# Kernel tuning notes

Hardware: AMD Instinct MI355X
Metric: run time of the kernel (lower is better)

The kernel has to match this reference:

```python
import jax, jax.numpy as jnp
import numpy as np

FISTA_ITER = 50
LAMBDA = 0.1
POWER_ITER = 100


def power_method(W):
    # Estimates c = largest eigenvalue of W^T W (squared spectral norm).
    # Torch code uses a random init vector; we use a fixed key for determinism.
    X0 = jax.random.normal(jax.random.key(1), (1, W.shape[1]), dtype=W.dtype)

    def body(i, carry):
        X, _ = carry
        X = (X @ W.T) @ W            # [1, m]
        nm = jnp.linalg.norm(X)
        return (X / nm, nm)

    _, nm = jax.lax.fori_loop(0, POWER_ITER, body, (X0, jnp.asarray(1.0, W.dtype)))
    return nm


def soft_threshold(X, lam):
    return jnp.sign(X) * jax.nn.relu(jnp.abs(X) - lam)


def fista(Y, W, lam, iters):
    c = power_method(W)
    eta = 1.0 / c
    Gamma0 = soft_threshold(Y @ (eta * W), lam)   # [B, m]
    Y_norm = jnp.linalg.norm(Y)
    t0 = jnp.asarray(1.0, Y.dtype)

    def step(carry, _):
        Gamma, Z, t = carry
        residual = Z @ W.T - Y                                   # [B, n]
        Gamma_new = soft_threshold(Z - eta * (residual @ W), lam / c)
        t_new = (1.0 + jnp.sqrt(1.0 + 4.0 * t ** 2)) / 2.0
        Z_new = Gamma_new + (t - 1.0) / t_new * (Gamma_new - Gamma)
        nrm = jnp.linalg.norm(residual) / Y_norm
        return (Gamma_new, Z_new, t_new), nrm

    (Gamma, _, _), norms = jax.lax.scan(step, (Gamma0, Gamma0, t0), None, length=iters)
    return Gamma, norms


def setup_inputs() -> dict:
    key = jax.random.key(0)
    k1, k2 = jax.random.split(key)
    Y = jax.random.normal(k1, (8192, 784), dtype=jnp.float32)
    W = jax.random.normal(k2, (784, 2048), dtype=jnp.float32)
    W = W / jnp.linalg.norm(W, axis=0, keepdims=True)  # NormDict
    return {"Y": Y, "W": W}


def reference(Y, W):
    Gamma, norms = fista(Y, W, LAMBDA, FISTA_ITER)
    X = Gamma @ W.T                  # reconstruction [B, 784]
    return (X, Gamma, norms)
```

## Files before the change

kernel.cpp:

```cpp
#include <hip/hip_runtime.h>
#include <math.h>

#define B_DIM   8192
#define N_DIM   784
#define NPAD    800
#define NROWS_W 1024
#define M_DIM   2048
#define XSZ     (B_DIM*N_DIM)
#define GSZ     (B_DIM*M_DIM)
#define NITER   50
#define PITER   100

typedef __attribute__((ext_vector_type(8))) short short8;
typedef __attribute__((ext_vector_type(4))) float floatx4;

__device__ __forceinline__ void async_ld16(const unsigned short* g, unsigned short* l){
  __builtin_amdgcn_global_load_lds(
      (const __attribute__((address_space(1))) unsigned int*)g,
      (__attribute__((address_space(3))) unsigned int*)l,
      16, 0, 0);
}

__device__ __forceinline__ unsigned rotl32(unsigned x, int d){ return (x<<d)|(x>>(32-d)); }

__device__ void threefry2x32(unsigned& v0, unsigned& v1){
  const unsigned ks0=0u, ks1=1u, ks2=0x1BD11BDBu;
  unsigned x0=v0+ks0, x1=v1+ks1;
#define RND(R) { x0+=x1; x1=rotl32(x1,R); x1^=x0; }
  RND(13) RND(15) RND(26) RND(6)
  x0+=ks1; x1+=ks2+1u;
  RND(17) RND(29) RND(16) RND(24)
  x0+=ks2; x1+=ks0+2u;
  RND(13) RND(15) RND(26) RND(6)
  x0+=ks0; x1+=ks1+3u;
  RND(17) RND(29) RND(16) RND(24)
  x0+=ks1; x1+=ks2+4u;
  RND(13) RND(15) RND(26) RND(6)
  x0+=ks2; x1+=ks0+5u;
#undef RND
  v0=x0; v1=x1;
}

__device__ float erfinv_f(float x){
  float w = -logf((1.0f-x)*(1.0f+x));
  float p;
  if (w < 5.0f){
    w -= 2.5f;
    p = 2.81022636e-08f;
    p = fmaf(p,w, 3.43273939e-07f);
    p = fmaf(p,w,-3.5233877e-06f);
    p = fmaf(p,w,-4.39150654e-06f);
    p = fmaf(p,w, 0.00021858087f);
    p = fmaf(p,w,-0.00125372503f);
    p = fmaf(p,w,-0.00417768164f);
    p = fmaf(p,w, 0.246640727f);
    p = fmaf(p,w, 1.50140941f);
  } else {
    w = sqrtf(w) - 3.0f;
    p = -0.000200214257f;
    p = fmaf(p,w, 0.000100950558f);
    p = fmaf(p,w, 0.00134934322f);
    p = fmaf(p,w,-0.00367342844f);
    p = fmaf(p,w, 0.00573950773f);
    p = fmaf(p,w,-0.0076224613f);
    p = fmaf(p,w, 0.00943887047f);
    p = fmaf(p,w, 1.00167406f);
    p = fmaf(p,w, 2.83297682f);
  }
  return p*x;
}

__device__ float bits_to_normal(unsigned b){
  unsigned fb = (b>>9) | 0x3f800000u;
  float u01 = __uint_as_float(fb) - 1.0f;
  const float lo = -0.99999994f;
  float u = u01*(1.0f - lo) + lo;
  u = fmaxf(lo, u);
  return 1.41421356237f * erfinv_f(u);
}

__global__ void setup_kernel(float* __restrict__ xbuf0, float* __restrict__ accs){
  int i = threadIdx.x;
  if (i < 64) accs[i] = 0.0f;
  unsigned v0 = (unsigned)i, v1 = (unsigned)(1024+i);
  threefry2x32(v0, v1);
  xbuf0[i]        = bits_to_normal(v0);
  xbuf0[1024 + i] = bits_to_normal(v1);
}

__device__ __forceinline__ unsigned short f2bf(float f){
  unsigned u = __float_as_uint(f);
  unsigned r = (u + 0x7fffu + ((u>>16)&1u)) >> 16;
  return (unsigned short)r;
}
__device__ __forceinline__ unsigned pack2(float a, float b){
  return (unsigned)f2bf(a) | ((unsigned)f2bf(b) << 16);
}
__device__ __forceinline__ float bf2f(unsigned short s){
  return __uint_as_float(((unsigned)s) << 16);
}

__global__ void conv_w(const float* __restrict__ W, unsigned short* __restrict__ Wbf){
  int i4 = (blockIdx.x*256 + threadIdx.x)*4;
  int row = i4 >> 11;
  uint2 p = make_uint2(0,0);
  if (row < N_DIM){
    float4 v = *(const float4*)(W + (size_t)row*M_DIM + (i4 & 2047));
    p.x = pack2(v.x, v.y); p.y = pack2(v.z, v.w);
  }
  *(uint2*)(Wbf + i4) = p;
}

__global__ void conv_y(const float* __restrict__ Y, unsigned short* __restrict__ Ybf){
  int row = blockIdx.x;
  int c4 = threadIdx.x*4;
  if (c4 >= NPAD) return;
  uint2 p = make_uint2(0,0);
  if (c4 < N_DIM){
    float4 v = *(const float4*)(Y + (size_t)row*N_DIM + c4);
    p.x = pack2(v.x, v.y); p.y = pack2(v.z, v.w);
  }
  *(uint2*)(Ybf + (size_t)row*NPAD + c4) = p;
}

__global__ void transpose_w(const float* __restrict__ W, unsigned short* __restrict__ WTbf){
  __shared__ float tile[32][33];
  int k0 = blockIdx.x*32;
  int j0 = blockIdx.y*32;
  int tx = threadIdx.x & 31, ty = threadIdx.x >> 5;
#pragma unroll
  for (int i=0;i<4;i++){
    int j = j0 + ty + 8*i;
    float v = (j < N_DIM) ? W[(size_t)j*M_DIM + k0 + tx] : 0.0f;
    tile[tx][ty+8*i] = v;
  }
  __syncthreads();
#pragma unroll
  for (int i=0;i<4;i++){
    int k = k0 + ty + 8*i;
    WTbf[(size_t)k*NPAD + j0 + tx] = f2bf(tile[ty+8*i][tx]);
  }
}

__global__ __launch_bounds__(256)
void compute_q(const float* __restrict__ W, float* __restrict__ Q){
  __shared__ float As2[16][132];
  __shared__ float Bs2[16][132];
  const int t = threadIdx.x;
  const int a0 = blockIdx.x*128, b0 = blockIdx.y*128;
  const int ty = t>>4, tx = t&15;
  float acc[8][8];
#pragma unroll
  for (int i=0;i<8;i++)
#pragma unroll
    for (int j=0;j<8;j++) acc[i][j]=0.0f;

  for (int j0=0; j0<N_DIM; j0+=16){
#pragma unroll
    for (int h=0; h<8; ++h){
      int idx = h*256 + t;
      int r = idx>>7, c = idx&127;
      As2[r][c] = W[(size_t)(j0+r)*M_DIM + a0 + c];
      Bs2[r][c] = W[(size_t)(j0+r)*M_DIM + b0 + c];
    }
    __syncthreads();
#pragma unroll
    for (int kk=0; kk<16; ++kk){
      float a[8], b[8];
#pragma unroll
      for (int i=0;i<8;i++) a[i] = As2[kk][ty*8+i];
#pragma unroll
      for (int j=0;j<8;j++) b[j] = Bs2[kk][tx*8+j];
#pragma unroll
      for (int i=0;i<8;i++)
#pragma unroll
        for (int j=0;j<8;j++) acc[i][j] = fmaf(a[i], b[j], acc[i][j]);
    }
    __syncthreads();
  }
#pragma unroll
  for (int i=0;i<8;i++){
    int a = a0 + ty*8 + i;
#pragma unroll
    for (int j=0;j<8;j++) Q[(size_t)a*M_DIM + b0 + tx*8 + j] = acc[i][j];
  }
}

__global__ void sumsq_kernel(const float* __restrict__ v, int n, float* __restrict__ acc){
  __shared__ float red[256];
  int t = threadIdx.x;
  float s = 0.0f;
  for (int i = blockIdx.x*256 + t; i < n; i += gridDim.x*256){ float x = v[i]; s = fmaf(x,x,s); }
  red[t] = s; __syncthreads();
  for (int off=128; off>0; off>>=1){ if (t<off) red[t]+=red[t+off]; __syncthreads(); }
  if (t==0) atomicAdd(acc, red[0]);
}

__global__ void pm_q(const float* __restrict__ x, const float* __restrict__ Q,
                     float* __restrict__ xout){
  __shared__ float red[256];
  int t = threadIdx.x;
  float s = 0.0f;
  for (int k=t; k<M_DIM; k+=256){ float v = x[k]; s = fmaf(v,v,s); }
  red[t]=s; __syncthreads();
  for (int off=128; off>0; off>>=1){ if (t<off) red[t]+=red[t+off]; __syncthreads(); }
  float inv = 1.0f/sqrtf(red[0]);
  int wave = t>>6, lane = t&63;
  int j = blockIdx.x*4 + wave;
  const float* Qr = Q + (size_t)j*M_DIM;
  float acc = 0.0f;
  for (int k=lane; k<M_DIM; k+=64) acc = fmaf(x[k], Qr[k], acc);
  for (int off=32; off>0; off>>=1) acc += __shfl_down(acc, off);
  if (lane==0) xout[j] = acc * inv;
}

__global__ void finish_power(const float* __restrict__ xfin, const float* __restrict__ accs,
                             float* __restrict__ params){
  __shared__ float red[256];
  int t = threadIdx.x;
  float s = 0.0f;
  for (int k=t; k<M_DIM; k+=256){ float v = xfin[k]; s = fmaf(v,v,s); }
  red[t]=s; __syncthreads();
  for (int off=128; off>0; off>>=1){ if (t<off) red[t]+=red[t+off]; __syncthreads(); }
  if (t==0){
    float c = sqrtf(red[0]);
    params[0] = c;
    params[1] = 1.0f/c;
    params[2] = 0.1f/c;
    params[3] = sqrtf(accs[0]);
  }
}

__device__ __forceinline__ float softthr(float v, float th){
  float a = fmaxf(fabsf(v) - th, 0.0f);
  return copysignf(a, v);
}

template<int MODE>
__global__ __launch_bounds__(256)
void mfma_nt(const unsigned short* __restrict__ Abf,
             const unsigned short* __restrict__ Bbf,
             const float* __restrict__ Y,
             unsigned short* __restrict__ Rbf,
             float* __restrict__ X,
             float* __restrict__ nacc){
  __shared__ float4 smem4[1280];
  unsigned short* As = (unsigned short*)smem4;
  unsigned short* Bs = As + 64*32;
  float* fbuf = (float*)smem4;

  const int bid = blockIdx.x;
  const int g8  = bid & 7, w = bid >> 3;
  const int m0  = (g8*16 + (w>>2))*64;
  const int n0  = (w & 3)*256;

  const int t    = threadIdx.x;
  const int wave = t>>6, lane = t&63;
  const int wm2  = wave>>1, wn2 = wave&1;
  const int quad = lane>>4, l15 = lane&15;
  const int lrow = lane>>2;
  const int lk   = (lane&3)*8;

  floatx4 acc[2][8];
#pragma unroll
  for (int i=0;i<2;i++)
#pragma unroll
    for (int j=0;j<8;j++) acc[i][j] = (floatx4)(0.0f);

  for (int k0=0; k0<M_DIM; k0+=32){
    async_ld16(Abf + (size_t)(m0 + wave*16 + lrow)*M_DIM + k0 + lk, &As[wave*512]);
#pragma unroll
    for (int c=0; c<4; ++c){
      int chunk = wave*4 + c;
      async_ld16(Bbf + (size_t)(n0 + chunk*16 + lrow)*M_DIM + k0 + lk, &Bs[chunk*512]);
    }
    __syncthreads();
    short8 af[2], bfr[8];
#pragma unroll
    for (int ti=0; ti<2; ++ti)
      af[ti] = *(const short8*)&As[(wm2*32 + ti*16 + l15)*32 + quad*8];
#pragma unroll
    for (int tj=0; tj<8; ++tj)
      bfr[tj] = *(const short8*)&Bs[(wn2*128 + tj*16 + l15)*32 + quad*8];
#pragma unroll
    for (int ti=0; ti<2; ++ti)
#pragma unroll
      for (int tj=0; tj<8; ++tj)
        acc[ti][tj] = __builtin_amdgcn_mfma_f32_16x16x32_bf16(af[ti], bfr[tj], acc[ti][tj], 0, 0, 0);
    __syncthreads();
  }

  float ss = 0.0f;
#pragma unroll
  for (int c=0; c<4; ++c){
    if (wn2 == (c>>1)){
      int tb = (c&1)*4;
#pragma unroll
      for (int ti=0; ti<2; ++ti)
#pragma unroll
        for (int u=0; u<4; ++u)
#pragma unroll
          for (int r=0; r<4; ++r)
            fbuf[(wm2*32 + ti*16 + quad*4 + r)*64 + u*16 + l15] = acc[ti][tb+u][r];
    }
    __syncthreads();
#pragma unroll
    for (int k=0; k<4; ++k){
      int row = k*16 + (t>>4);
      int col = (t&15)*4;
      int m = m0 + row;
      int n = n0 + c*64 + col;
      float4 v = *(const float4*)&fbuf[row*64 + col];
      if (MODE==0){
        if (n < N_DIM){
          float4 yv = *(const float4*)(Y + (size_t)m*N_DIM + n);
          float r0 = v.x - yv.x, r1 = v.y - yv.y, r2 = v.z - yv.z, r3 = v.w - yv.w;
          uint2 p; p.x = pack2(r0, r1); p.y = pack2(r2, r3);
          *(uint2*)(Rbf + (size_t)m*NPAD + n) = p;
          ss = fmaf(r0,r0, fmaf(r1,r1, fmaf(r2,r2, fmaf(r3,r3, ss))));
        } else if (n < NPAD){
          *(uint2*)(Rbf + (size_t)m*NPAD + n) = make_uint2(0,0);
        }
      } else {
        if (n < N_DIM) *(float4*)(X + (size_t)m*N_DIM + n) = v;
      }
    }
    __syncthreads();
  }

  if (MODE==0){
    for (int off=32; off>0; off>>=1) ss += __shfl_down(ss, off);
    if (lane==0) atomicAdd(nacc, ss);
  }
}

template<int MODE>
__global__ __launch_bounds__(256)
void mfma_nn(const unsigned short* __restrict__ Abf,
             const unsigned short* __restrict__ WTbf,
             float* __restrict__ Gamma,
             unsigned short* __restrict__ Zhi,
             unsigned short* __restrict__ Zlo,
             const float* __restrict__ params,
             float mu){
  __shared__ float4 smem4[1536];
  unsigned short* As = (unsigned short*)smem4;
  unsigned short* Bs = As + 128*32;
  float* fbuf = (float*)smem4;

  const int bid = blockIdx.x;
  const int g8  = bid & 7, w = bid >> 3;
  const int m0  = (g8*8 + (w>>3))*128;
  const int n0  = (w & 7)*256;

  const int t    = threadIdx.x;
  const int wave = t>>6, lane = t&63;
  const int wm   = wave>>1, wn = wave&1;
  const int quad = lane>>4, l15 = lane&15;
  const int lrow = lane>>2;
  const int lk   = (lane&3)*8;

  floatx4 acc[4][8];
#pragma unroll
  for (int i=0;i<4;i++)
#pragma unroll
    for (int j=0;j<8;j++) acc[i][j] = (floatx4)(0.0f);

  for (int k0=0; k0<NPAD; k0+=32){
#pragma unroll
    for (int c=0; c<2; ++c){
      int chunk = wave*2 + c;
      async_ld16(Abf + (size_t)(m0 + chunk*16 + lrow)*NPAD + k0 + lk, &As[chunk*512]);
    }
#pragma unroll
    for (int c=0; c<4; ++c){
      int chunk = wave*4 + c;
      async_ld16(WTbf + (size_t)(n0 + chunk*16 + lrow)*NPAD + k0 + lk, &Bs[chunk*512]);
    }
    __syncthreads();
    short8 af[4], bfr[8];
#pragma unroll
    for (int ti=0; ti<4; ++ti)
      af[ti] = *(const short8*)&As[(wm*64 + ti*16 + l15)*32 + quad*8];
#pragma unroll
    for (int tj=0; tj<8; ++tj)
      bfr[tj] = *(const short8*)&Bs[(wn*128 + tj*16 + l15)*32 + quad*8];
#pragma unroll
    for (int ti=0; ti<4; ++ti)
#pragma unroll
      for (int tj=0; tj<8; ++tj)
        acc[ti][tj] = __builtin_amdgcn_mfma_f32_16x16x32_bf16(af[ti], bfr[tj], acc[ti][tj], 0, 0, 0);
    __syncthreads();
  }

  const float eta  = params[1];
  const float lamc = params[2];

#pragma unroll
  for (int c=0; c<8; ++c){
    if (wn == (c>>2)){
      int tb = (c&3)*2;
#pragma unroll
      for (int ti=0; ti<4; ++ti)
#pragma unroll
        for (int u=0; u<2; ++u)
#pragma unroll
          for (int r=0; r<4; ++r)
            fbuf[(wm*64 + ti*16 + quad*4 + r)*32 + u*16 + l15] = acc[ti][tb+u][r];
    }
    __syncthreads();
#pragma unroll
    for (int k=0; k<4; ++k){
      int row = k*32 + (t>>3);
      int col = (t&7)*4;
      int m = m0 + row;
      int n = n0 + c*32 + col;
      size_t idx = (size_t)m*M_DIM + n;
      float4 g4 = *(const float4*)&fbuf[row*32 + col];
      float gr[4] = {g4.x, g4.y, g4.z, g4.w};
      float go4[4];
      if (MODE!=0){
        uint2 ph = *(const uint2*)(Zhi + idx);
        uint2 pl = *(const uint2*)(Zlo + idx);
        unsigned short h[4] = {(unsigned short)(ph.x&0xffff),(unsigned short)(ph.x>>16),
                               (unsigned short)(ph.y&0xffff),(unsigned short)(ph.y>>16)};
        unsigned short l[4] = {(unsigned short)(pl.x&0xffff),(unsigned short)(pl.x>>16),
                               (unsigned short)(pl.y&0xffff),(unsigned short)(pl.y>>16)};
        float4 gov = *(const float4*)(Gamma + idx);
        go4[0]=gov.x; go4[1]=gov.y; go4[2]=gov.z; go4[3]=gov.w;
#pragma unroll
        for (int e=0;e<4;e++){
          float zv = bf2f(h[e]) + bf2f(l[e]);
          gr[e] = softthr(zv - eta*gr[e], lamc);
        }
      } else {
#pragma unroll
        for (int e=0;e<4;e++) gr[e] = softthr(eta*gr[e], 0.1f);
      }
      *(float4*)(Gamma + idx) = make_float4(gr[0],gr[1],gr[2],gr[3]);
      if (MODE==1){
        float zn[4];
#pragma unroll
        for (int e=0;e<4;e++) zn[e] = gr[e] + mu*(gr[e] - go4[e]);
        unsigned short h0=f2bf(zn[0]), h1=f2bf(zn[1]), h2=f2bf(zn[2]), h3=f2bf(zn[3]);
        uint2 ph; ph.x = (unsigned)h0 | ((unsigned)h1<<16); ph.y = (unsigned)h2 | ((unsigned)h3<<16);
        uint2 pl; pl.x = pack2(zn[0]-bf2f(h0), zn[1]-bf2f(h1));
                  pl.y = pack2(zn[2]-bf2f(h2), zn[3]-bf2f(h3));
        *(uint2*)(Zhi + idx) = ph;
        *(uint2*)(Zlo + idx) = pl;
      } else if (MODE==0){
        unsigned short h0=f2bf(gr[0]), h1=f2bf(gr[1]), h2=f2bf(gr[2]), h3=f2bf(gr[3]);
        uint2 ph; ph.x = (unsigned)h0 | ((unsigned)h1<<16); ph.y = (unsigned)h2 | ((unsigned)h3<<16);
        uint2 pl; pl.x = pack2(gr[0]-bf2f(h0), gr[1]-bf2f(h1));
                  pl.y = pack2(gr[2]-bf2f(h2), gr[3]-bf2f(h3));
        *(uint2*)(Zhi + idx) = ph;
        *(uint2*)(Zlo + idx) = pl;
      } else {
        uint2 ph; ph.x = pack2(gr[0], gr[1]); ph.y = pack2(gr[2], gr[3]);
        *(uint2*)(Zhi + idx) = ph;
      }
    }
    __syncthreads();
  }
}

__global__ void norms_finalize(const float* __restrict__ nacc, const float* __restrict__ params,
                               float* __restrict__ out){
  int i = threadIdx.x;
  if (i < NITER) out[i] = sqrtf(nacc[i]) / params[3];
}

extern "C" void kernel_launch(void* const* d_in, const int* in_sizes, int n_in,
                              void* d_out, int out_size, void* d_ws, size_t ws_size,
                              hipStream_t stream){
  const float* Y  = (const float*)d_in[0];
  const float* W  = (const float*)d_in[1];
  float* out      = (float*)d_out;
  float* X        = out;
  float* Gamma    = out + XSZ;
  float* norms    = out + XSZ + GSZ;

  unsigned short* Zhi  = (unsigned short*)d_ws;
  unsigned short* Zlo  = Zhi  + (size_t)GSZ;
  unsigned short* Rbf  = Zlo  + (size_t)GSZ;
  unsigned short* Wbf  = Rbf  + (size_t)B_DIM*NPAD;
  unsigned short* WTbf = Wbf  + (size_t)NROWS_W*M_DIM;
  float* Q      = (float*)(WTbf + (size_t)M_DIM*NPAD);
  float* xb0    = Q + (size_t)M_DIM*M_DIM;
  float* xb1    = xb0 + M_DIM;
  float* params = xb1 + M_DIM;
  float* accs   = params + 8;

  setup_kernel<<<dim3(1), dim3(1024), 0, stream>>>(xb0, accs);
  sumsq_kernel<<<dim3(512), dim3(256), 0, stream>>>(Y, XSZ, accs);
  conv_w      <<<dim3(2048), dim3(256), 0, stream>>>(W, Wbf);
  transpose_w <<<dim3(64,25), dim3(256), 0, stream>>>(W, WTbf);
  conv_y      <<<dim3(B_DIM), dim3(256), 0, stream>>>(Y, Rbf);

  compute_q<<<dim3(16,16), dim3(256), 0, stream>>>(W, Q);
  float* xa = xb0; float* xc = xb1;
  for (int it=0; it<PITER; ++it){
    pm_q<<<dim3(512), dim3(256), 0, stream>>>(xa, Q, xc);
    float* tmp = xa; xa = xc; xc = tmp;
  }
  finish_power<<<dim3(1), dim3(256), 0, stream>>>(xa, accs, params);

  mfma_nn<0><<<dim3(512), dim3(256), 0, stream>>>(Rbf, WTbf, Gamma, Zhi, Zlo, params, 0.0f);

  float tcur = 1.0f;
  for (int it=0; it<NITER; ++it){
    mfma_nt<0><<<dim3(512), dim3(256), 0, stream>>>(Zhi, Wbf, Y, Rbf, nullptr, accs + 1 + it);
    float tsq = tcur*tcur;
    float tn  = (1.0f + sqrtf(1.0f + 4.0f*tsq)) / 2.0f;
    float mu  = (tcur - 1.0f) / tn;
    tcur = tn;
    if (it < NITER-1)
      mfma_nn<1><<<dim3(512), dim3(256), 0, stream>>>(Rbf, WTbf, Gamma, Zhi, Zlo, params, mu);
    else
      mfma_nn<2><<<dim3(512), dim3(256), 0, stream>>>(Rbf, WTbf, Gamma, Zhi, Zlo, params, mu);
  }

  norms_finalize<<<dim3(1), dim3(64), 0, stream>>>(accs + 1, params, norms);

  mfma_nt<1><<<dim3(512), dim3(256), 0, stream>>>(Zhi, Wbf, nullptr, nullptr, X, nullptr);
}
```

Before: 9.269 ms.

## Double-buffer LDS tiles in both GEMMs and shrink mfma_nn tile for more blocks

```diff
diff --git a/kernel.cpp b/kernel.cpp
--- a/kernel.cpp
+++ b/kernel.cpp
@@ -244,9 +244,11 @@
              unsigned short* __restrict__ Rbf,
              float* __restrict__ X,
              float* __restrict__ nacc){
-  __shared__ float4 smem4[1280];
-  unsigned short* As = (unsigned short*)smem4;
-  unsigned short* Bs = As + 64*32;
+  __shared__ float4 smem4[2560];
+  unsigned short* As0 = (unsigned short*)smem4;
+  unsigned short* Bs0 = As0 + 64*32;
+  unsigned short* As1 = Bs0 + 256*32;
+  unsigned short* Bs1 = As1 + 64*32;
   float* fbuf = (float*)smem4;
 
   const int bid = blockIdx.x;
@@ -267,14 +269,22 @@
 #pragma unroll
     for (int j=0;j<8;j++) acc[i][j] = (floatx4)(0.0f);
 
-  for (int k0=0; k0<M_DIM; k0+=32){
+  auto stage = [&](unsigned short* As, unsigned short* Bs, int k0){
     async_ld16(Abf + (size_t)(m0 + wave*16 + lrow)*M_DIM + k0 + lk, &As[wave*512]);
 #pragma unroll
     for (int c=0; c<4; ++c){
       int chunk = wave*4 + c;
       async_ld16(Bbf + (size_t)(n0 + chunk*16 + lrow)*M_DIM + k0 + lk, &Bs[chunk*512]);
     }
-    __syncthreads();
+  };
+
+  stage(As0, Bs0, 0);
+  __syncthreads();
+  int cur = 0;
+  for (int k0=0; k0<M_DIM; k0+=32, cur^=1){
+    unsigned short* As = cur ? As1 : As0;
+    unsigned short* Bs = cur ? Bs1 : Bs0;
+    if (k0+32 < M_DIM) stage(cur ? As0 : As1, cur ? Bs0 : Bs1, k0+32);
     short8 af[2], bfr[8];
 #pragma unroll
     for (int ti=0; ti<2; ++ti)
@@ -301,7 +311,7 @@
         for (int u=0; u<4; ++u)
 #pragma unroll
           for (int r=0; r<4; ++r)
-            fbuf[(wm2*32 + ti*16 + quad*4 + r)*64 + u*16 + l15] = acc[ti][tb+u][r];
+            fbuf[(wm2*32 + ti*16 + quad*4 + r)*68 + u*16 + l15] = acc[ti][tb+u][r];
     }
     __syncthreads();
 #pragma unroll
@@ -310,7 +320,7 @@
       int col = (t&15)*4;
       int m = m0 + row;
       int n = n0 + c*64 + col;
-      float4 v = *(const float4*)&fbuf[row*64 + col];
+      float4 v = *(const float4*)&fbuf[row*68 + col];
       if (MODE==0){
         if (n < N_DIM){
           float4 yv = *(const float4*)(Y + (size_t)m*N_DIM + n);
@@ -335,7 +345,7 @@
 }
 
 template<int MODE>
-__global__ __launch_bounds__(256)
+__global__ __launch_bounds__(256,3)
 void mfma_nn(const unsigned short* __restrict__ Abf,
              const unsigned short* __restrict__ WTbf,
              float* __restrict__ Gamma,
@@ -343,15 +353,17 @@
              unsigned short* __restrict__ Zlo,
              const float* __restrict__ params,
              float mu){
-  __shared__ float4 smem4[1536];
-  unsigned short* As = (unsigned short*)smem4;
-  unsigned short* Bs = As + 128*32;
+  __shared__ float4 smem4[2048];
+  unsigned short* As0 = (unsigned short*)smem4;
+  unsigned short* Bs0 = As0 + 128*32;
+  unsigned short* As1 = Bs0 + 128*32;
+  unsigned short* Bs1 = As1 + 128*32;
   float* fbuf = (float*)smem4;
 
   const int bid = blockIdx.x;
   const int g8  = bid & 7, w = bid >> 3;
-  const int m0  = (g8*8 + (w>>3))*128;
-  const int n0  = (w & 7)*256;
+  const int m0  = (g8*8 + (w>>4))*128;
+  const int n0  = (w & 15)*128;
 
   const int t    = threadIdx.x;
   const int wave = t>>6, lane = t&63;
@@ -360,35 +372,39 @@
   const int lrow = lane>>2;
   const int lk   = (lane&3)*8;
 
-  floatx4 acc[4][8];
+  floatx4 acc[4][4];
 #pragma unroll
   for (int i=0;i<4;i++)
 #pragma unroll
-    for (int j=0;j<8;j++) acc[i][j] = (floatx4)(0.0f);
-
-  for (int k0=0; k0<NPAD; k0+=32){
+    for (int j=0;j<4;j++) acc[i][j] = (floatx4)(0.0f);
+
+  auto stage = [&](unsigned short* As, unsigned short* Bs, int k0){
 #pragma unroll
     for (int c=0; c<2; ++c){
       int chunk = wave*2 + c;
-      async_ld16(Abf + (size_t)(m0 + chunk*16 + lrow)*NPAD + k0 + lk, &As[chunk*512]);
-    }
-#pragma unroll
-    for (int c=0; c<4; ++c){
-      int chunk = wave*4 + c;
+      async_ld16(Abf  + (size_t)(m0 + chunk*16 + lrow)*NPAD + k0 + lk, &As[chunk*512]);
       async_ld16(WTbf + (size_t)(n0 + chunk*16 + lrow)*NPAD + k0 + lk, &Bs[chunk*512]);
     }
-    __syncthreads();
-    short8 af[4], bfr[8];
+  };
+
+  stage(As0, Bs0, 0);
+  __syncthreads();
+  int cur = 0;
+  for (int k0=0; k0<NPAD; k0+=32, cur^=1){
+    unsigned short* As = cur ? As1 : As0;
+    unsigned short* Bs = cur ? Bs1 : Bs0;
+    if (k0+32 < NPAD) stage(cur ? As0 : As1, cur ? Bs0 : Bs1, k0+32);
+    short8 af[4], bfr[4];
 #pragma unroll
     for (int ti=0; ti<4; ++ti)
       af[ti] = *(const short8*)&As[(wm*64 + ti*16 + l15)*32 + quad*8];
 #pragma unroll
-    for (int tj=0; tj<8; ++tj)
-      bfr[tj] = *(const short8*)&Bs[(wn*128 + tj*16 + l15)*32 + quad*8];
+    for (int tj=0; tj<4; ++tj)
+      bfr[tj] = *(const short8*)&Bs[(wn*64 + tj*16 + l15)*32 + quad*8];
 #pragma unroll
     for (int ti=0; ti<4; ++ti)
 #pragma unroll
-      for (int tj=0; tj<8; ++tj)
+      for (int tj=0; tj<4; ++tj)
         acc[ti][tj] = __builtin_amdgcn_mfma_f32_16x16x32_bf16(af[ti], bfr[tj], acc[ti][tj], 0, 0, 0);
     __syncthreads();
   }
@@ -397,37 +413,44 @@
   const float lamc = params[2];
 
 #pragma unroll
-  for (int c=0; c<8; ++c){
-    if (wn == (c>>2)){
-      int tb = (c&3)*2;
+  for (int c=0; c<4; ++c){
+    if (wn == (c>>1)){
+      int tb = (c&1)*2;
 #pragma unroll
       for (int ti=0; ti<4; ++ti)
 #pragma unroll
         for (int u=0; u<2; ++u)
 #pragma unroll
           for (int r=0; r<4; ++r)
-            fbuf[(wm*64 + ti*16 + quad*4 + r)*32 + u*16 + l15] = acc[ti][tb+u][r];
-    }
-    __syncthreads();
+            fbuf[(wm*64 + ti*16 + quad*4 + r)*36 + u*16 + l15] = acc[ti][tb+u][r];
+    }
+    __syncthreads();
+    const int rbase = t>>3;
+    const int col   = (t&7)*4;
+    const int n     = n0 + c*32 + col;
+    size_t idx[4];
+    uint2 ph[4], pl[4];
+    float4 gov[4];
 #pragma unroll
     for (int k=0; k<4; ++k){
-      int row = k*32 + (t>>3);
-      int col = (t&7)*4;
-      int m = m0 + row;
-      int n = n0 + c*32 + col;
-      size_t idx = (size_t)m*M_DIM + n;
-      float4 g4 = *(const float4*)&fbuf[row*32 + col];
+      int m = m0 + k*32 + rbase;
+      idx[k] = (size_t)m*M_DIM + n;
+      if (MODE!=0){
+        ph[k] = *(const uint2*)(Zhi + idx[k]);
+        pl[k] = *(const uint2*)(Zlo + idx[k]);
+      }
+      if (MODE==1) gov[k] = *(const float4*)(Gamma + idx[k]);
+    }
+#pragma unroll
+    for (int k=0; k<4; ++k){
+      int row = k*32 + rbase;
+      float4 g4 = *(const float4*)&fbuf[row*36 + col];
       float gr[4] = {g4.x, g4.y, g4.z, g4.w};
-      float go4[4];
       if (MODE!=0){
-        uint2 ph = *(const uint2*)(Zhi + idx);
-        uint2 pl = *(const uint2*)(Zlo + idx);
-        unsigned short h[4] = {(unsigned short)(ph.x&0xffff),(unsigned short)(ph.x>>16),
-                               (unsigned short)(ph.y&0xffff),(unsigned short)(ph.y>>16)};
-        unsigned short l[4] = {(unsigned short)(pl.x&0xffff),(unsigned short)(pl.x>>16),
-                               (unsigned short)(pl.y&0xffff),(unsigned short)(pl.y>>16)};
-        float4 gov = *(const float4*)(Gamma + idx);
-        go4[0]=gov.x; go4[1]=gov.y; go4[2]=gov.z; go4[3]=gov.w;
+        unsigned short h[4] = {(unsigned short)(ph[k].x&0xffff),(unsigned short)(ph[k].x>>16),
+                               (unsigned short)(ph[k].y&0xffff),(unsigned short)(ph[k].y>>16)};
+        unsigned short l[4] = {(unsigned short)(pl[k].x&0xffff),(unsigned short)(pl[k].x>>16),
+                               (unsigned short)(pl[k].y&0xffff),(unsigned short)(pl[k].y>>16)};
 #pragma unroll
         for (int e=0;e<4;e++){
           float zv = bf2f(h[e]) + bf2f(l[e]);
@@ -437,27 +460,30 @@
 #pragma unroll
         for (int e=0;e<4;e++) gr[e] = softthr(eta*gr[e], 0.1f);
       }
-      *(float4*)(Gamma + idx) = make_float4(gr[0],gr[1],gr[2],gr[3]);
+      *(float4*)(Gamma + idx[k]) = make_float4(gr[0],gr[1],gr[2],gr[3]);
       if (MODE==1){
+        float go0 = gov[k].x, go1 = gov[k].y, go2 = gov[k].z, go3 = gov[k].w;
         float zn[4];
-#pragma unroll
-        for (int e=0;e<4;e++) zn[e] = gr[e] + mu*(gr[e] - go4[e]);
+        zn[0] = gr[0] + mu*(gr[0] - go0);
+        zn[1] = gr[1] + mu*(gr[1] - go1);
+        zn[2] = gr[2] + mu*(gr[2] - go2);
+        zn[3] = gr[3] + mu*(gr[3] - go3);
         unsigned short h0=f2bf(zn[0]), h1=f2bf(zn[1]), h2=f2bf(zn[2]), h3=f2bf(zn[3]);
-        uint2 ph; ph.x = (unsigned)h0 | ((unsigned)h1<<16); ph.y = (unsigned)h2 | ((unsigned)h3<<16);
-        uint2 pl; pl.x = pack2(zn[0]-bf2f(h0), zn[1]-bf2f(h1));
-                  pl.y = pack2(zn[2]-bf2f(h2), zn[3]-bf2f(h3));
-        *(uint2*)(Zhi + idx) = ph;
-        *(uint2*)(Zlo + idx) = pl;
+        uint2 phx; phx.x = (unsigned)h0 | ((unsigned)h1<<16); phx.y = (unsigned)h2 | ((unsigned)h3<<16);
+        uint2 plx; plx.x = pack2(zn[0]-bf2f(h0), zn[1]-bf2f(h1));
+                   plx.y = pack2(zn[2]-bf2f(h2), zn[3]-bf2f(h3));
+        *(uint2*)(Zhi + idx[k]) = phx;
+        *(uint2*)(Zlo + idx[k]) = plx;
       } else if (MODE==0){
         unsigned short h0=f2bf(gr[0]), h1=f2bf(gr[1]), h2=f2bf(gr[2]), h3=f2bf(gr[3]);
-        uint2 ph; ph.x = (unsigned)h0 | ((unsigned)h1<<16); ph.y = (unsigned)h2 | ((unsigned)h3<<16);
-        uint2 pl; pl.x = pack2(gr[0]-bf2f(h0), gr[1]-bf2f(h1));
-                  pl.y = pack2(gr[2]-bf2f(h2), gr[3]-bf2f(h3));
-        *(uint2*)(Zhi + idx) = ph;
-        *(uint2*)(Zlo + idx) = pl;
+        uint2 phx; phx.x = (unsigned)h0 | ((unsigned)h1<<16); phx.y = (unsigned)h2 | ((unsigned)h3<<16);
+        uint2 plx; plx.x = pack2(gr[0]-bf2f(h0), gr[1]-bf2f(h1));
+                   plx.y = pack2(gr[2]-bf2f(h2), gr[3]-bf2f(h3));
+        *(uint2*)(Zhi + idx[k]) = phx;
+        *(uint2*)(Zlo + idx[k]) = plx;
       } else {
-        uint2 ph; ph.x = pack2(gr[0], gr[1]); ph.y = pack2(gr[2], gr[3]);
-        *(uint2*)(Zhi + idx) = ph;
+        uint2 phx; phx.x = pack2(gr[0], gr[1]); phx.y = pack2(gr[2], gr[3]);
+        *(uint2*)(Zhi + idx[k]) = phx;
       }
     }
     __syncthreads();
@@ -505,7 +531,7 @@
   }
   finish_power<<<dim3(1), dim3(256), 0, stream>>>(xa, accs, params);
 
-  mfma_nn<0><<<dim3(512), dim3(256), 0, stream>>>(Rbf, WTbf, Gamma, Zhi, Zlo, params, 0.0f);
+  mfma_nn<0><<<dim3(1024), dim3(256), 0, stream>>>(Rbf, WTbf, Gamma, Zhi, Zlo, params, 0.0f);
 
   float tcur = 1.0f;
   for (int it=0; it<NITER; ++it){
@@ -515,9 +541,9 @@
     float mu  = (tcur - 1.0f) / tn;
     tcur = tn;
     if (it < NITER-1)
-      mfma_nn<1><<<dim3(512), dim3(256), 0, stream>>>(Rbf, WTbf, Gamma, Zhi, Zlo, params, mu);
+      mfma_nn<1><<<dim3(1024), dim3(256), 0, stream>>>(Rbf, WTbf, Gamma, Zhi, Zlo, params, mu);
     else
-      mfma_nn<2><<<dim3(512), dim3(256), 0, stream>>>(Rbf, WTbf, Gamma, Zhi, Zlo, params, mu);
+      mfma_nn<2><<<dim3(1024), dim3(256), 0, stream>>>(Rbf, WTbf, Gamma, Zhi, Zlo, params, mu);
   }
 
   norms_finalize<<<dim3(1), dim3(64), 0, stream>>>(accs + 1, params, norms);
```

Measured after the change: 8.316 ms. 1.11x faster.
